# Optimization experiments

Measured on AMD Instinct MI355X. Metric: run time of the kernel, lower is better.

Reference implementation:

```python
import jax, jax.numpy as jnp
import numpy as np

N_EMBD = 1024
N_HEAD = 16
HEAD_DIM = N_EMBD // N_HEAD


def setup_inputs() -> dict:
    key = jax.random.key(0)
    ks = jax.random.split(key, 9)
    B, T, C = 4, 2048, N_EMBD
    s = 1.0 / np.sqrt(C)
    return {
        "x": jax.random.normal(ks[0], (B, T, C), jnp.float32),
        "Wq": jax.random.normal(ks[1], (C, C), jnp.float32) * s,
        "bq": jnp.zeros((C,), jnp.float32),
        "Wk": jax.random.normal(ks[2], (C, C), jnp.float32) * s,
        "bk": jnp.zeros((C,), jnp.float32),
        "Wv": jax.random.normal(ks[3], (C, C), jnp.float32) * s,
        "bv": jnp.zeros((C,), jnp.float32),
        "Wp": jax.random.normal(ks[4], (C, C), jnp.float32) * s,
        "bp": jnp.zeros((C,), jnp.float32),
    }


def reference(x, Wq, bq, Wk, bk, Wv, bv, Wp, bp):
    B, T, C = x.shape
    H, D = N_HEAD, HEAD_DIM
    # QKV projections -> (B, H, T, D)
    q = (x @ Wq + bq).reshape(B, T, H, D).transpose(0, 2, 1, 3)
    k = (x @ Wk + bk).reshape(B, T, H, D).transpose(0, 2, 1, 3)
    v = (x @ Wv + bv).reshape(B, T, H, D).transpose(0, 2, 1, 3)
    # scaled scores with causal mask
    att = jnp.einsum("bhtd,bhsd->bhts", q, k) / jnp.sqrt(jnp.asarray(D, x.dtype))
    causal = jnp.tril(jnp.ones((T, T), bool))
    att = jnp.where(causal, att, jnp.asarray(-jnp.inf, att.dtype))
    att = jax.nn.softmax(att, axis=-1)
    # dropout is identity in eval/reference mode
    out = jnp.einsum("bhts,bhsd->bhtd", att, v)
    out = out.transpose(0, 2, 1, 3).reshape(B, T, C)
    return out @ Wp + bp
```

## Files before the change

### kernel.cpp

```cpp
#include <hip/hip_runtime.h>
#include <stdint.h>


typedef __attribute__((ext_vector_type(8))) short bf16x8;
typedef __attribute__((ext_vector_type(8))) ushort u16x8;
typedef __attribute__((ext_vector_type(4))) float f32x4;

__device__ __forceinline__ ushort f2bf(float f) {
  union { float f; uint32_t i; } c; c.f = f;
  uint32_t r = c.i + 0x7fffu + ((c.i >> 16) & 1u);
  return (ushort)(r >> 16);
}
__device__ __forceinline__ uint32_t cvt_pk_bf16(float lo, float hi) {
  uint32_t r;
  asm("v_cvt_pk_bf16_f32 %0, %1, %2" : "=v"(r) : "v"(lo), "v"(hi));
  return r;
}

#define GLOAD16(gp, lp)                                                          \
  __builtin_amdgcn_global_load_lds(                                              \
      (const __attribute__((address_space(1))) unsigned int*)(gp),               \
      (__attribute__((address_space(3))) unsigned int*)(lp), 16, 0, 0)

#define SCQ 0.1803368801111204f

__global__ __launch_bounds__(256) void f32_to_bf16(const float* __restrict__ in,
                                                   ushort* __restrict__ out, int n) {
  const int i = (blockIdx.x * 256 + threadIdx.x) * 8;
  if (i + 8 > n) return;
  float4 a = *(const float4*)(in + i);
  float4 b = *(const float4*)(in + i + 4);
  u16x8 r;
  r[0] = f2bf(a.x); r[1] = f2bf(a.y); r[2] = f2bf(a.z); r[3] = f2bf(a.w);
  r[4] = f2bf(b.x); r[5] = f2bf(b.y); r[6] = f2bf(b.z); r[7] = f2bf(b.w);
  *(u16x8*)(out + i) = r;
}

__global__ __launch_bounds__(256) void transpose4_f32_bf16(
    const float* __restrict__ Wq, const float* __restrict__ Wk,
    const float* __restrict__ Wv, const float* __restrict__ Wp,
    const float* __restrict__ bq, const float* __restrict__ bk,
    const float* __restrict__ bv,
    ushort* __restrict__ wt, float* __restrict__ bcat) {
  const int z = blockIdx.z;
  const float* W = (z == 0) ? Wq : (z == 1) ? Wk : (z == 2) ? Wv : Wp;
  ushort* Wt = wt + (size_t)z * 1024 * 1024;
  __shared__ ushort tile[32][33];
  const int k0 = blockIdx.x * 32, n0 = blockIdx.y * 32;
  const int tx = threadIdx.x & 31, ty = threadIdx.x >> 5;
#pragma unroll
  for (int i = 0; i < 4; ++i)
    tile[ty + i * 8][tx] = f2bf(W[(size_t)(k0 + ty + i * 8) * 1024 + n0 + tx]);
  __syncthreads();
#pragma unroll
  for (int i = 0; i < 4; ++i)
    Wt[(size_t)(n0 + ty + i * 8) * 1024 + k0 + tx] = tile[tx][ty + i * 8];
  if (z < 3 && blockIdx.x == 0 && blockIdx.y == 0) {
    const float* bs = (z == 0) ? bq : (z == 1) ? bk : bv;
    for (int i = threadIdx.x; i < 1024; i += 256) bcat[z * 1024 + i] = bs[i];
  }
}

template <int MODE>
__global__ __launch_bounds__(256) void gemm_bt(const ushort* __restrict__ A,
                                               const ushort* __restrict__ Bt,
                                               const float* __restrict__ bias,
                                               void* __restrict__ outp,
                                               int M, int N, int K) {
  __shared__ ushort As[3][128][32];
  __shared__ ushort Bs[3][128][32];
  const int tid = threadIdx.x;
  const int lane = tid & 63, wave = tid >> 6;
  const int quad = lane >> 4, l16 = lane & 15;
  const int wy = wave >> 1, wx = wave & 1;
  const int m0 = blockIdx.x * 128, n0 = blockIdx.y * 128;

  const f32x4 fzero = {0.f, 0.f, 0.f, 0.f};
  f32x4 acc[4][4];
#pragma unroll
  for (int i = 0; i < 4; ++i)
#pragma unroll
    for (int j = 0; j < 4; ++j) acc[i][j] = fzero;

  const int r = lane >> 2, ch = (lane & 3) * 8;
  const ushort* Abase = A + (size_t)(m0 + wave * 32 + r) * K + ch;
  const ushort* Bbase = Bt + (size_t)(n0 + wave * 32 + r) * K + ch;

#define STAGE_GEMM(buf, kt)                                                \
  do {                                                                     \
    GLOAD16(Abase + (kt) * 32,          &As[buf][wave * 32][0]);           \
    GLOAD16(Abase + 16 * K + (kt) * 32, &As[buf][wave * 32 + 16][0]);      \
    GLOAD16(Bbase + (kt) * 32,          &Bs[buf][wave * 32][0]);           \
    GLOAD16(Bbase + 16 * K + (kt) * 32, &Bs[buf][wave * 32 + 16][0]);      \
  } while (0)

  STAGE_GEMM(0, 0);
  STAGE_GEMM(1, 1);

  const int nk = K >> 5;
  int cur = 0;
  for (int kt = 0; kt < nk; ++kt) {
    if (kt < nk - 1) asm volatile("s_waitcnt vmcnt(4)" ::: "memory");
    else             asm volatile("s_waitcnt vmcnt(0)" ::: "memory");
    __builtin_amdgcn_s_barrier();
    __builtin_amdgcn_sched_barrier(0);

    if (kt + 2 < nk) {
      int nb = cur + 2; if (nb >= 3) nb -= 3;
      STAGE_GEMM(nb, kt + 2);
    }

    bf16x8 af[4], bfr[4];
#pragma unroll
    for (int i = 0; i < 4; ++i)
      af[i] = *(const bf16x8*)&As[cur][wy * 64 + i * 16 + l16][quad * 8];
#pragma unroll
    for (int j = 0; j < 4; ++j)
      bfr[j] = *(const bf16x8*)&Bs[cur][wx * 64 + j * 16 + l16][quad * 8];
#pragma unroll
    for (int i = 0; i < 4; ++i)
#pragma unroll
      for (int j = 0; j < 4; ++j)
        acc[i][j] = __builtin_amdgcn_mfma_f32_16x16x32_bf16(af[i], bfr[j], acc[i][j], 0, 0, 0);

    cur = (cur == 2) ? 0 : cur + 1;
  }
#undef STAGE_GEMM

#pragma unroll
  for (int j = 0; j < 4; ++j) {
    const int col = n0 + wx * 64 + j * 16 + l16;
    const float bv = bias[col];
#pragma unroll
    for (int i = 0; i < 4; ++i) {
#pragma unroll
      for (int rr = 0; rr < 4; ++rr) {
        const int row = m0 + wy * 64 + i * 16 + quad * 4 + rr;
        float v = acc[i][j][rr] + bv;
        if (MODE == 0) {
          ((float*)outp)[(size_t)row * N + col] = v;
        } else {
          ushort* out = (ushort*)outp;
          const int g = col >> 10, cc = col & 1023;
          const int b = row >> 11, t = row & 2047, h = cc >> 6, d = cc & 63;
          if (g == 0) v *= SCQ;
          const size_t go = (size_t)g * 8192 * 1024;
          size_t idx;
          if (g == 2) idx = go + (((size_t)(b * 16 + h) * 64) + d) * 2048 + t;
          else        idx = go + (((size_t)(b * 16 + h) * 2048) + t) * 64 + d;
          out[idx] = f2bf(v);
        }
      }
    }
  }
}

__global__ __launch_bounds__(256, 3) void attn_kernel(const ushort* __restrict__ q,
                                                      const ushort* __restrict__ k,
                                                      const ushort* __restrict__ v,
                                                      ushort* __restrict__ y) {
  const int T = 2048;
  const int bh = blockIdx.x;
  const int qt = 15 - (int)blockIdx.y;
  const int qbase = qt * 128;
  const int tid = threadIdx.x;
  const int lane = tid & 63, wave = tid >> 6;
  const int quad = lane >> 4, l16 = lane & 15;
  const int rr = lane >> 3, c8 = lane & 7;
  const int swz = l16 & 7;

  __shared__ ushort Ks[2][64][64];
  __shared__ ushort Vs[2][64][64];
  __shared__ ushort Ps[4][16][64];

  const ushort* qp = q + (size_t)bh * T * 64;
  const ushort* kp = k + (size_t)bh * T * 64;
  const ushort* vp = v + (size_t)bh * 64 * T;
  const int b = bh >> 4, h = bh & 15;

  bf16x8 aq[2][2];
#pragma unroll
  for (int i = 0; i < 2; ++i)
#pragma unroll
    for (int kk = 0; kk < 2; ++kk)
      aq[i][kk] = *(const bf16x8*)(qp + (size_t)(qbase + wave * 32 + i * 16 + l16) * 64 +
                                   kk * 32 + quad * 8);

  const f32x4 fzero = {0.f, 0.f, 0.f, 0.f};
  f32x4 acc_o[2][4];
  float lstate[2];
#pragma unroll
  for (int i = 0; i < 2; ++i) {
    lstate[i] = 0.f;
#pragma unroll
    for (int jd = 0; jd < 4; ++jd) acc_o[i][jd] = fzero;
  }

  const int trow0 = qbase + wave * 32;
  const int nkt = qt * 2 + 2;

#pragma unroll
  for (int t = 0; t < 2; ++t) {
    const int row = wave * 16 + t * 8 + rr;
    const int gc = c8 ^ (row & 7);
    GLOAD16(kp + (size_t)row * 64 + gc * 8, &Ks[0][wave * 16 + t * 8][0]);
    GLOAD16(vp + (size_t)row * T + gc * 8,  &Vs[0][wave * 16 + t * 8][0]);
  }
  __syncthreads();

  ushort* prow = &Ps[wave][l16][0];

  int cur = 0;
  for (int kt = 0; kt < nkt; ++kt) {
    if (kt + 1 < nkt) {
#pragma unroll
      for (int t = 0; t < 2; ++t) {
        const int row = wave * 16 + t * 8 + rr;
        const int gc = c8 ^ (row & 7);
        GLOAD16(kp + (size_t)((kt + 1) * 64 + row) * 64 + gc * 8,
                &Ks[cur ^ 1][wave * 16 + t * 8][0]);
        GLOAD16(vp + (size_t)row * T + (kt + 1) * 64 + gc * 8,
                &Vs[cur ^ 1][wave * 16 + t * 8][0]);
      }
    }

    if (!(kt * 64 > trow0 + 31)) {
      bf16x8 ak[4][2];
#pragma unroll
      for (int j = 0; j < 4; ++j)
#pragma unroll
        for (int kk = 0; kk < 2; ++kk)
          ak[j][kk] = *(const bf16x8*)&Ks[cur][j * 16 + l16][((4 * kk + quad) ^ swz) * 8];

#pragma unroll
      for (int i = 0; i < 2; ++i) {
        const int tmin = trow0 + i * 16;
        if (kt * 64 > tmin + 15) continue;
        const int tglob = tmin + l16;

        f32x4 st[4];
#pragma unroll
        for (int j = 0; j < 4; ++j) st[j] = fzero;
#pragma unroll
        for (int j = 0; j < 4; ++j)
#pragma unroll
          for (int kk = 0; kk < 2; ++kk)
            st[j] = __builtin_amdgcn_mfma_f32_16x16x32_bf16(ak[j][kk], aq[i][kk], st[j], 0, 0, 0);

        float rs = 0.f;
        const bool needmask = (kt * 64 + 63 > tmin);
        if (needmask) {
#pragma unroll
          for (int j = 0; j < 4; ++j)
#pragma unroll
            for (int r2 = 0; r2 < 4; ++r2) {
              const int sg = kt * 64 + j * 16 + quad * 4 + r2;
              const float xv = (sg > tglob) ? -1e30f : st[j][r2];
              const float p = exp2f(xv);
              st[j][r2] = p;
              rs += p;
            }
        } else {
#pragma unroll
          for (int j = 0; j < 4; ++j)
#pragma unroll
            for (int r2 = 0; r2 < 4; ++r2) {
              const float p = exp2f(st[j][r2]);
              st[j][r2] = p;
              rs += p;
            }
        }
        rs += __shfl_xor(rs, 16, 64);
        rs += __shfl_xor(rs, 32, 64);
        lstate[i] += rs;

#pragma unroll
        for (int j = 0; j < 4; ++j) {
          uint2 w2;
          w2.x = cvt_pk_bf16(st[j][0], st[j][1]);
          w2.y = cvt_pk_bf16(st[j][2], st[j][3]);
          const int cb = 2 * j + (quad >> 1);
          *(uint2*)(prow + ((cb ^ swz) << 3) + ((quad & 1) << 2)) = w2;
        }
        bf16x8 pb0 = *(const bf16x8*)(prow + ((quad ^ swz) << 3));
        bf16x8 pb1 = *(const bf16x8*)(prow + (((4 + quad) ^ swz) << 3));

#pragma unroll
        for (int jd = 0; jd < 4; ++jd) {
          const int vrow = jd * 16 + l16;
          bf16x8 av0 = *(const bf16x8*)&Vs[cur][vrow][((quad) ^ swz) * 8];
          bf16x8 av1 = *(const bf16x8*)&Vs[cur][vrow][((4 + quad) ^ swz) * 8];
          acc_o[i][jd] = __builtin_amdgcn_mfma_f32_16x16x32_bf16(av0, pb0, acc_o[i][jd], 0, 0, 0);
          acc_o[i][jd] = __builtin_amdgcn_mfma_f32_16x16x32_bf16(av1, pb1, acc_o[i][jd], 0, 0, 0);
        }
      }
    }

    __syncthreads();
    cur ^= 1;
  }

#pragma unroll
  for (int i = 0; i < 2; ++i) {
    const int t = trow0 + i * 16 + l16;
    const float inv = 1.0f / lstate[i];
#pragma unroll
    for (int jd = 0; jd < 4; ++jd) {
      uint2 w;
      w.x = cvt_pk_bf16(acc_o[i][jd][0] * inv, acc_o[i][jd][1] * inv);
      w.y = cvt_pk_bf16(acc_o[i][jd][2] * inv, acc_o[i][jd][3] * inv);
      *(uint2*)&y[((size_t)(b * 2048 + t)) * 1024 + h * 64 + jd * 16 + quad * 4] = w;
    }
  }
}

extern "C" void kernel_launch(void* const* d_in, const int* in_sizes, int n_in,
                              void* d_out, int out_size, void* d_ws, size_t ws_size,
                              hipStream_t stream) {
  const float* x  = (const float*)d_in[0];
  const float* Wq = (const float*)d_in[1];
  const float* bq = (const float*)d_in[2];
  const float* Wk = (const float*)d_in[3];
  const float* bk = (const float*)d_in[4];
  const float* Wv = (const float*)d_in[5];
  const float* bv = (const float*)d_in[6];
  const float* Wp = (const float*)d_in[7];
  const float* bp = (const float*)d_in[8];

  ushort* ws  = (ushort*)d_ws;
  ushort* wqt = ws;
  ushort* wpt = wqt + (size_t)3 * 1024 * 1024;
  ushort* xb  = wpt + (size_t)1024 * 1024;
  ushort* qq  = xb + (size_t)8192 * 1024;
  ushort* kk  = qq + (size_t)8192 * 1024;
  ushort* vv  = kk + (size_t)8192 * 1024;
  ushort* y   = vv + (size_t)8192 * 1024;
  float*  bcat = (float*)(y + (size_t)8192 * 1024);

  const dim3 tb(256);
  hipLaunchKernelGGL(f32_to_bf16, dim3(4096), tb, 0, stream, x, xb, 8192 * 1024);
  hipLaunchKernelGGL(transpose4_f32_bf16, dim3(32, 32, 4), tb, 0, stream,
                     Wq, Wk, Wv, Wp, bq, bk, bv, wqt, bcat);

  hipLaunchKernelGGL((gemm_bt<3>), dim3(64, 24), tb, 0, stream,
                     xb, wqt, bcat, (void*)qq, 8192, 3072, 1024);

  const dim3 ag(64, 16);
  hipLaunchKernelGGL(attn_kernel, ag, tb, 0, stream, qq, kk, vv, y);

  hipLaunchKernelGGL((gemm_bt<0>), dim3(64, 8), tb, 0, stream,
                     y, wpt, bp, d_out, 8192, 1024, 1024);
}
```

Before: 287.5 us.

## Add 256x256-tile 8-wave QKV GEMM with swizzled LDS and ping-pong schedule

Replaces the 128x128 QKV projection GEMM with a dedicated 512-thread kernel using 256x256 output tiles. It double-buffers LDS loads with XOR swizzling and interleaves direct-to-LDS loads with MFMA phases behind explicit barriers and s_setprio. The goal is more operand reuse per loaded byte and better overlap of memory and matrix work. The cost is higher register pressure (8x4 accumulators per wave), a grid of only 384 blocks, and more fragile hand-tuned waitcnt/barrier ordering.

```diff
diff --git a/kernel.cpp b/kernel.cpp
--- a/kernel.cpp
+++ b/kernel.cpp
@@ -61,11 +61,174 @@
   }
 }
 
-template <int MODE>
+__global__ __launch_bounds__(512) void gemm_qkv8(const ushort* __restrict__ A,
+                                                 const ushort* __restrict__ Bt,
+                                                 const float* __restrict__ bias,
+                                                 ushort* __restrict__ out) {
+  __shared__ ushort As[2][2][256][32];
+  __shared__ ushort Bs[2][2][256][32];
+  const int K = 1024;
+  const int tid = threadIdx.x;
+  const int lane = tid & 63, wave = tid >> 6;
+  const int wm = wave >> 2, wn = wave & 3;
+  const int quad = lane >> 4, l16 = lane & 15;
+  const int m0 = blockIdx.x * 256, n0 = blockIdx.y * 256;
+
+  const int srow = lane >> 2;
+  const int sslot = (lane & 3) ^ ((lane >> 3) & 3);
+  const ushort* Asrc = A + (size_t)(m0 + wm * 128 + wn * 32 + srow) * K + sslot * 8;
+  const ushort* Bsrc = Bt + (size_t)(n0 + wn * 64 + wm * 32 + srow) * K + sslot * 8;
+  const int rslot8 = (quad ^ ((l16 >> 1) & 3)) * 8;
+
+#define STAGE_A8(buf, kk, kt)                                                   \
+  do {                                                                          \
+    GLOAD16(Asrc + (size_t)(kt) * 64 + (kk) * 32,                               \
+            &As[buf][kk][wm * 128 + wn * 32][0]);                               \
+    GLOAD16(Asrc + (size_t)16 * K + (size_t)(kt) * 64 + (kk) * 32,              \
+            &As[buf][kk][wm * 128 + wn * 32 + 16][0]);                          \
+  } while (0)
+#define STAGE_B8(buf, kk, kt)                                                   \
+  do {                                                                          \
+    GLOAD16(Bsrc + (size_t)(kt) * 64 + (kk) * 32,                               \
+            &Bs[buf][kk][wn * 64 + wm * 32][0]);                                \
+    GLOAD16(Bsrc + (size_t)16 * K + (size_t)(kt) * 64 + (kk) * 32,              \
+            &Bs[buf][kk][wn * 64 + wm * 32 + 16][0]);                           \
+  } while (0)
+
+  const f32x4 fzero = {0.f, 0.f, 0.f, 0.f};
+  f32x4 acc[8][4];
+#pragma unroll
+  for (int i = 0; i < 8; ++i)
+#pragma unroll
+    for (int j = 0; j < 4; ++j) acc[i][j] = fzero;
+
+  STAGE_A8(0, 0, 0);
+  STAGE_B8(0, 0, 0);
+  __builtin_amdgcn_sched_barrier(0);
+  STAGE_A8(0, 1, 0);
+  STAGE_B8(0, 1, 0);
+  asm volatile("s_waitcnt vmcnt(4)" ::: "memory");
+  __builtin_amdgcn_sched_barrier(0);
+  __builtin_amdgcn_s_barrier();
+
+  const int nt = 16;
+  for (int kt = 0; kt < nt; ++kt) {
+    const int b = kt & 1, nb = b ^ 1;
+    const bool more = (kt + 1 < nt);
+    bf16x8 aA[4], aB[4];
+
+#pragma unroll
+    for (int i = 0; i < 4; ++i)
+      aA[i] = *(const bf16x8*)&As[b][0][wm * 128 + i * 16 + l16][rslot8];
+#pragma unroll
+    for (int j = 0; j < 4; ++j)
+      aB[j] = *(const bf16x8*)&Bs[b][0][wn * 64 + j * 16 + l16][rslot8];
+    if (more) STAGE_A8(nb, 0, kt + 1);
+    __builtin_amdgcn_sched_barrier(0);
+    __builtin_amdgcn_s_barrier();
+    asm volatile("s_waitcnt lgkmcnt(0)" ::: "memory");
+    __builtin_amdgcn_sched_barrier(0);
+    __builtin_amdgcn_s_setprio(1);
+#pragma unroll
+    for (int i = 0; i < 4; ++i)
+#pragma unroll
+      for (int j = 0; j < 4; ++j)
+        acc[i][j] = __builtin_amdgcn_mfma_f32_16x16x32_bf16(aA[i], aB[j], acc[i][j], 0, 0, 0);
+    __builtin_amdgcn_s_setprio(0);
+    __builtin_amdgcn_sched_barrier(0);
+    __builtin_amdgcn_s_barrier();
+
+#pragma unroll
+    for (int i = 0; i < 4; ++i)
+      aA[i] = *(const bf16x8*)&As[b][0][wm * 128 + (4 + i) * 16 + l16][rslot8];
+    if (more) STAGE_B8(nb, 0, kt + 1);
+    __builtin_amdgcn_sched_barrier(0);
+    __builtin_amdgcn_s_barrier();
+    asm volatile("s_waitcnt lgkmcnt(0)" ::: "memory");
+    __builtin_amdgcn_sched_barrier(0);
+    __builtin_amdgcn_s_setprio(1);
+#pragma unroll
+    for (int i = 0; i < 4; ++i)
+#pragma unroll
+      for (int j = 0; j < 4; ++j)
+        acc[4 + i][j] = __builtin_amdgcn_mfma_f32_16x16x32_bf16(aA[i], aB[j], acc[4 + i][j], 0, 0, 0);
+    __builtin_amdgcn_s_setprio(0);
+    if (more) asm volatile("s_waitcnt vmcnt(4)" ::: "memory");
+    else      asm volatile("s_waitcnt vmcnt(0)" ::: "memory");
+    __builtin_amdgcn_sched_barrier(0);
+    __builtin_amdgcn_s_barrier();
+
+#pragma unroll
+    for (int i = 0; i < 4; ++i)
+      aA[i] = *(const bf16x8*)&As[b][1][wm * 128 + i * 16 + l16][rslot8];
+#pragma unroll
+    for (int j = 0; j < 4; ++j)
+      aB[j] = *(const bf16x8*)&Bs[b][1][wn * 64 + j * 16 + l16][rslot8];
+    if (more) STAGE_A8(nb, 1, kt + 1);
+    __builtin_amdgcn_sched_barrier(0);
+    __builtin_amdgcn_s_barrier();
+    asm volatile("s_waitcnt lgkmcnt(0)" ::: "memory");
+    __builtin_amdgcn_sched_barrier(0);
+    __builtin_amdgcn_s_setprio(1);
+#pragma unroll
+    for (int i = 0; i < 4; ++i)
+#pragma unroll
+      for (int j = 0; j < 4; ++j)
+        acc[i][j] = __builtin_amdgcn_mfma_f32_16x16x32_bf16(aA[i], aB[j], acc[i][j], 0, 0, 0);
+    __builtin_amdgcn_s_setprio(0);
+    __builtin_amdgcn_sched_barrier(0);
+    __builtin_amdgcn_s_barrier();
+
+#pragma unroll
+    for (int i = 0; i < 4; ++i)
+      aA[i] = *(const bf16x8*)&As[b][1][wm * 128 + (4 + i) * 16 + l16][rslot8];
+    if (more) STAGE_B8(nb, 1, kt + 1);
+    __builtin_amdgcn_sched_barrier(0);
+    __builtin_amdgcn_s_barrier();
+    asm volatile("s_waitcnt lgkmcnt(0)" ::: "memory");
+    __builtin_amdgcn_sched_barrier(0);
+    __builtin_amdgcn_s_setprio(1);
+#pragma unroll
+    for (int i = 0; i < 4; ++i)
+#pragma unroll
+      for (int j = 0; j < 4; ++j)
+        acc[4 + i][j] = __builtin_amdgcn_mfma_f32_16x16x32_bf16(aA[i], aB[j], acc[4 + i][j], 0, 0, 0);
+    __builtin_amdgcn_s_setprio(0);
+    if (more) asm volatile("s_waitcnt vmcnt(4)" ::: "memory");
+    __builtin_amdgcn_sched_barrier(0);
+    __builtin_amdgcn_s_barrier();
+  }
+#undef STAGE_A8
+#undef STAGE_B8
+
+#pragma unroll
+  for (int ms = 0; ms < 8; ++ms) {
+#pragma unroll
+    for (int ns = 0; ns < 4; ++ns) {
+      const int col = n0 + wn * 64 + ns * 16 + l16;
+      const int g = col >> 10, cc = col & 1023;
+      const int h = cc >> 6, d = cc & 63;
+      const float bv = bias[col];
+      const size_t go = (size_t)g * 8192 * 1024;
+#pragma unroll
+      for (int rr = 0; rr < 4; ++rr) {
+        const int row = m0 + wm * 128 + ms * 16 + quad * 4 + rr;
+        float v = acc[ms][ns][rr] + bv;
+        if (g == 0) v *= SCQ;
+        const int bb = row >> 11, t = row & 2047;
+        size_t idx;
+        if (g == 2) idx = go + (((size_t)(bb * 16 + h) * 64) + d) * 2048 + t;
+        else        idx = go + (((size_t)(bb * 16 + h) * 2048) + t) * 64 + d;
+        out[idx] = f2bf(v);
+      }
+    }
+  }
+}
+
 __global__ __launch_bounds__(256) void gemm_bt(const ushort* __restrict__ A,
                                                const ushort* __restrict__ Bt,
                                                const float* __restrict__ bias,
-                                               void* __restrict__ outp,
+                                               float* __restrict__ outp,
                                                int M, int N, int K) {
   __shared__ ushort As[3][128][32];
   __shared__ ushort Bs[3][128][32];
@@ -136,20 +299,7 @@
 #pragma unroll
       for (int rr = 0; rr < 4; ++rr) {
         const int row = m0 + wy * 64 + i * 16 + quad * 4 + rr;
-        float v = acc[i][j][rr] + bv;
-        if (MODE == 0) {
-          ((float*)outp)[(size_t)row * N + col] = v;
-        } else {
-          ushort* out = (ushort*)outp;
-          const int g = col >> 10, cc = col & 1023;
-          const int b = row >> 11, t = row & 2047, h = cc >> 6, d = cc & 63;
-          if (g == 0) v *= SCQ;
-          const size_t go = (size_t)g * 8192 * 1024;
-          size_t idx;
-          if (g == 2) idx = go + (((size_t)(b * 16 + h) * 64) + d) * 2048 + t;
-          else        idx = go + (((size_t)(b * 16 + h) * 2048) + t) * 64 + d;
-          out[idx] = f2bf(v);
-        }
+        outp[(size_t)row * N + col] = acc[i][j][rr] + bv;
       }
     }
   }
@@ -342,12 +492,12 @@
   hipLaunchKernelGGL(transpose4_f32_bf16, dim3(32, 32, 4), tb, 0, stream,
                      Wq, Wk, Wv, Wp, bq, bk, bv, wqt, bcat);
 
-  hipLaunchKernelGGL((gemm_bt<3>), dim3(64, 24), tb, 0, stream,
-                     xb, wqt, bcat, (void*)qq, 8192, 3072, 1024);
+  hipLaunchKernelGGL(gemm_qkv8, dim3(32, 12), dim3(512), 0, stream,
+                     xb, wqt, bcat, qq);
 
   const dim3 ag(64, 16);
   hipLaunchKernelGGL(attn_kernel, ag, tb, 0, stream, qq, kk, vv, y);
 
-  hipLaunchKernelGGL((gemm_bt<0>), dim3(64, 8), tb, 0, stream,
-                     y, wpt, bp, d_out, 8192, 1024, 1024);
-}
+  hipLaunchKernelGGL(gemm_bt, dim3(64, 8), tb, 0, stream,
+                     y, wpt, bp, (float*)d_out, 8192, 1024, 1024);
+}
```

Result: slower. 302.6 us (+5.3%).
